# Optimization experiments

Measured on AMD Instinct MI355X. Metric: run time of the kernel, lower is better.

Reference implementation:

```python
import jax, jax.numpy as jnp
import numpy as np
import math

HEADS, LANDMARKS, PINV_ITERS, RES_K = 8, 256, 6, 33
DIM = 512


def layer_norm(x, g, b, eps=1e-5):
    mu = x.mean(-1, keepdims=True)
    var = ((x - mu) ** 2).mean(-1, keepdims=True)
    return (x - mu) * jax.lax.rsqrt(var + eps) * g + b


def iter_pinv(x, iters=PINV_ITERS):
    # Moore-Penrose pseudo-inverse via Newton-Schulz-like iteration (lucidrains nystrom-attention)
    ax = jnp.abs(x)
    z = jnp.swapaxes(x, -1, -2) / (jnp.max(ax.sum(-1)) * jnp.max(ax.sum(-2)))
    I = jnp.eye(x.shape[-1], dtype=x.dtype)
    for _ in range(iters):
        xz = x @ z
        z = 0.25 * z @ (13.0 * I - xz @ (15.0 * I - xz @ (7.0 * I - xz)))
    return z


def nystrom_attention(x, qkv_w, out_w, out_b, res_w):
    b, n, dim = x.shape
    h, m = HEADS, LANDMARKS
    d = dim // h
    pad = (m - n % m) % m
    xp = jnp.pad(x, ((0, 0), (pad, 0), (0, 0)))  # pad at sequence start (as in original)
    npad = n + pad
    qkv = xp @ qkv_w  # [b, npad, 3*dim]
    q, k, v = jnp.split(qkv, 3, axis=-1)
    q, k, v = (t.reshape(b, npad, h, d).transpose(0, 2, 1, 3) for t in (q, k, v))
    q = q * (d ** -0.5)
    l = npad // m
    q_l = q.reshape(b, h, m, l, d).mean(3)  # [b,h,m,d] landmarks
    k_l = k.reshape(b, h, m, l, d).mean(3)
    attn1 = jax.nn.softmax(jnp.einsum('bhid,bhjd->bhij', q, k_l), axis=-1)    # [b,h,npad,m]
    attn2 = jax.nn.softmax(jnp.einsum('bhid,bhjd->bhij', q_l, k_l), axis=-1)  # [b,h,m,m]
    attn3 = jax.nn.softmax(jnp.einsum('bhid,bhjd->bhij', q_l, k), axis=-1)    # [b,h,m,npad]
    out = (attn1 @ iter_pinv(attn2)) @ (attn3 @ v)  # [b,h,npad,d]
    # depthwise residual conv over sequence dim: v as NCHW = [b, heads, npad, d], kernel (33,1)
    res = jax.lax.conv_general_dilated(
        v, res_w, window_strides=(1, 1), padding=((RES_K // 2, RES_K // 2), (0, 0)),
        dimension_numbers=('NCHW', 'OIHW', 'NCHW'), feature_group_count=h)
    out = out + res
    out = out.transpose(0, 2, 1, 3).reshape(b, npad, dim)
    out = out @ out_w + out_b  # dropout is identity at eval
    return out[:, -n:]


def dwconv(x, w, b, k):
    y = jax.lax.conv_general_dilated(
        x, w, (1, 1), ((k // 2, k // 2), (k // 2, k // 2)),
        dimension_numbers=('NCHW', 'OIHW', 'NCHW'), feature_group_count=x.shape[1])
    return y + b[None, :, None, None]


def ppeg(x, H, W, w7, b7, w5, b5, w3, b3):
    B, _, C = x.shape
    cls_tok, feat = x[:, :1], x[:, 1:]
    cnn = feat.transpose(0, 2, 1).reshape(B, C, H, W)
    y = cnn + dwconv(cnn, w7, b7, 7) + dwconv(cnn, w5, b5, 5) + dwconv(cnn, w3, b3, 3)
    y = y.reshape(B, C, H * W).transpose(0, 2, 1)
    return jnp.concatenate([cls_tok, y], axis=1)


def _forward(features, fc1_w, fc1_b, cls_token,
             l1_norm_g, l1_norm_b, l1_qkv_w, l1_out_w, l1_out_b, l1_res_w,
             ppeg_w7, ppeg_b7, ppeg_w5, ppeg_b5, ppeg_w3, ppeg_b3,
             l2_norm_g, l2_norm_b, l2_qkv_w, l2_out_w, l2_out_b, l2_res_w,
             norm_g, norm_b, fc2_w, fc2_b):
    h = jax.nn.relu(features @ fc1_w + fc1_b)  # [B, N, 512]
    B, N, D = h.shape
    _H = _W = int(math.ceil(math.sqrt(N)))
    add_length = _H * _W - N
    h = jnp.concatenate([h, h[:, :add_length, :]], axis=1)  # square pad by wraparound
    h = jnp.concatenate([jnp.broadcast_to(cls_token, (B, 1, D)), h], axis=1)
    h = h + nystrom_attention(layer_norm(h, l1_norm_g, l1_norm_b), l1_qkv_w, l1_out_w, l1_out_b, l1_res_w)
    h = ppeg(h, _H, _W, ppeg_w7, ppeg_b7, ppeg_w5, ppeg_b5, ppeg_w3, ppeg_b3)
    h = h + nystrom_attention(layer_norm(h, l2_norm_g, l2_norm_b), l2_qkv_w, l2_out_w, l2_out_b, l2_res_w)
    h = layer_norm(h, norm_g, norm_b)[:, 0]
    return h @ fc2_w + fc2_b  # [B, num_classes]


def setup_inputs() -> dict:
    key = jax.random.key(0)
    ks = jax.random.split(key, 32)
    B, N, F, D = 2, 16000, 1024, DIM
    s = 0.02
    def rn(k, shape, scale=s):
        return jax.random.normal(k, shape, dtype=jnp.float32) * scale
    inp = {
        'features': jax.random.normal(ks[0], (B, N, F), dtype=jnp.float32),
        'fc1_w': rn(ks[1], (F, D)), 'fc1_b': jnp.zeros((D,), jnp.float32),
        'cls_token': rn(ks[2], (1, 1, D), 1.0),
        'l1_norm_g': jnp.ones((D,), jnp.float32), 'l1_norm_b': jnp.zeros((D,), jnp.float32),
        'l1_qkv_w': rn(ks[3], (D, 3 * D)),
        'l1_out_w': rn(ks[4], (D, D)), 'l1_out_b': jnp.zeros((D,), jnp.float32),
        'l1_res_w': rn(ks[5], (HEADS, 1, RES_K, 1)),
        'ppeg_w7': rn(ks[6], (D, 1, 7, 7)), 'ppeg_b7': jnp.zeros((D,), jnp.float32),
        'ppeg_w5': rn(ks[7], (D, 1, 5, 5)), 'ppeg_b5': jnp.zeros((D,), jnp.float32),
        'ppeg_w3': rn(ks[8], (D, 1, 3, 3)), 'ppeg_b3': jnp.zeros((D,), jnp.float32),
        'l2_norm_g': jnp.ones((D,), jnp.float32), 'l2_norm_b': jnp.zeros((D,), jnp.float32),
        'l2_qkv_w': rn(ks[9], (D, 3 * D)),
        'l2_out_w': rn(ks[10], (D, D)), 'l2_out_b': jnp.zeros((D,), jnp.float32),
        'l2_res_w': rn(ks[11], (HEADS, 1, RES_K, 1)),
        'norm_g': jnp.ones((D,), jnp.float32), 'norm_b': jnp.zeros((D,), jnp.float32),
        'fc2_w': rn(ks[12], (D, 1)), 'fc2_b': jnp.zeros((1,), jnp.float32),
    }
    return inp


def reference(features, fc1_w, fc1_b, cls_token,
              l1_norm_g, l1_norm_b, l1_qkv_w, l1_out_w, l1_out_b, l1_res_w,
              ppeg_w7, ppeg_b7, ppeg_w5, ppeg_b5, ppeg_w3, ppeg_b3,
              l2_norm_g, l2_norm_b, l2_qkv_w, l2_out_w, l2_out_b, l2_res_w,
              norm_g, norm_b, fc2_w, fc2_b):
    return _forward(features, fc1_w, fc1_b, cls_token,
                    l1_norm_g, l1_norm_b, l1_qkv_w, l1_out_w, l1_out_b, l1_res_w,
                    ppeg_w7, ppeg_b7, ppeg_w5, ppeg_b5, ppeg_w3, ppeg_b3,
                    l2_norm_g, l2_norm_b, l2_qkv_w, l2_out_w, l2_out_b, l2_res_w,
                    norm_g, norm_b, fc2_w, fc2_b)
```

## Files before the change

### kernel.cpp

```cpp
#include <hip/hip_runtime.h>
#include <math.h>

#define NTOK 16130
#define NPAD 16384
#define PADF 254
#define NB   2
#define DM   512
#define NH   8
#define HD   64
#define LM   256
#define SEG  64

typedef __attribute__((ext_vector_type(8))) short short8v;
typedef __attribute__((ext_vector_type(4))) float f32x4;

__device__ __forceinline__ float wred_max(float v){
  #pragma unroll
  for(int o=32;o;o>>=1) v=fmaxf(v,__shfl_xor(v,o));
  return v;
}
__device__ __forceinline__ float wred_sum(float v){
  #pragma unroll
  for(int o=32;o;o>>=1) v+=__shfl_xor(v,o);
  return v;
}
__device__ __forceinline__ float block_max256(float v, float* s4){
  v=wred_max(v);
  if((threadIdx.x&63)==0) s4[threadIdx.x>>6]=v;
  __syncthreads();
  v=fmaxf(fmaxf(s4[0],s4[1]),fmaxf(s4[2],s4[3]));
  __syncthreads();
  return v;
}
__device__ __forceinline__ float block_sum256(float v, float* s4){
  v=wred_sum(v);
  if((threadIdx.x&63)==0) s4[threadIdx.x>>6]=v;
  __syncthreads();
  v=s4[0]+s4[1]+s4[2]+s4[3];
  __syncthreads();
  return v;
}
__device__ __forceinline__ unsigned short f2bf(float f){
  unsigned u=__float_as_uint(f);
  u = u + 0x7FFFu + ((u>>16)&1u);
  return (unsigned short)(u>>16);
}
__device__ __forceinline__ float bf2f(unsigned short u){
  return __uint_as_float(((unsigned)u)<<16);
}
__device__ __forceinline__ unsigned cvtpk(float a, float b){
  unsigned r;
  asm("v_cvt_pk_bf16_f32 %0, %1, %2" : "=v"(r) : "v"(a), "v"(b));
  return r;
}

__global__ void k_wconv_t(const float* __restrict__ W, unsigned short* __restrict__ Wt,
                          int K, int N){
  int idx=blockIdx.x*256+threadIdx.x; if(idx>=K*N) return;
  int k=idx/N, n=idx%N;
  Wt[(size_t)n*K+k]=f2bf(W[idx]);
}

template<int MODE, int ASRC>
__global__ __launch_bounds__(256) void k_mfma_gemm(
    const void* __restrict__ Ap, const unsigned short* __restrict__ Bt,
    int M, int N, int K,
    const float* __restrict__ bias,
    void* __restrict__ o0, void* __restrict__ o1, void* __restrict__ o2)
{
  __shared__ unsigned short As[128*32];
  __shared__ unsigned short Bs[128*32];
  int t=threadIdx.x;
  int bx=blockIdx.x, by=blockIdx.y;
  {
    int gx=gridDim.x; int wg=by*gx+bx; int nwg=gx*gridDim.y;
    int cpx=nwg>>3; int x2=(wg&7)*cpx+(wg>>3);
    by=x2/gx; bx=x2-by*gx;
  }
  int row0=by*128, col0=bx*128;
  int lane=t&63, w=t>>6, wr=w>>1, wc=w&1, lr=lane&15, kg=lane>>4;
  f32x4 acc[4][4];
  #pragma unroll
  for(int m=0;m<4;m++)
    #pragma unroll
    for(int n=0;n<4;n++) acc[m][n]=(f32x4){0.f,0.f,0.f,0.f};

  auto loadA=[&](int r,int kofs)->short8v{
    if constexpr(ASRC==0){
      return *(const short8v*)((const unsigned short*)Ap+(size_t)(row0+r)*K+kofs);
    } else if constexpr(ASRC==1){
      const float* Af=(const float*)Ap;
      float4 f0=*(const float4*)(Af+(size_t)(row0+r)*K+kofs);
      float4 f1=*(const float4*)(Af+(size_t)(row0+r)*K+kofs+4);
      union{unsigned u[4]; short8v v;} pk;
      pk.u[0]=cvtpk(f0.x,f0.y); pk.u[1]=cvtpk(f0.z,f0.w);
      pk.u[2]=cvtpk(f1.x,f1.y); pk.u[3]=cvtpk(f1.z,f1.w);
      return pk.v;
    } else {
      const float* Af=(const float*)Ap;
      int rr2=row0+r; int bb=rr2>>14, ri=rr2&16383;
      int head=kofs>>6, dd=kofs&63;
      const float* p=Af + (((size_t)bb*NH+head)*NPAD+ri)*HD + dd;
      float4 f0=*(const float4*)p;
      float4 f1=*(const float4*)(p+4);
      union{unsigned u[4]; short8v v;} pk;
      pk.u[0]=cvtpk(f0.x,f0.y); pk.u[1]=cvtpk(f0.z,f0.w);
      pk.u[2]=cvtpk(f1.x,f1.y); pk.u[3]=cvtpk(f1.z,f1.w);
      return pk.v;
    }
  };

  short8v ra[2], rb[2];
  #pragma unroll
  for(int i=0;i<2;i++){
    int flat=i*256+t, r=flat>>2, k8=flat&3;
    ra[i]=loadA(r, k8*8);
    rb[i]=*(const short8v*)(Bt+(size_t)(col0+r)*K + k8*8);
  }
  int k0=0;
  for(;;){
    __syncthreads();
    #pragma unroll
    for(int i=0;i<2;i++){
      int flat=i*256+t;
      *(short8v*)(As+flat*8)=ra[i];
      *(short8v*)(Bs+flat*8)=rb[i];
    }
    __syncthreads();
    k0+=32;
    if(k0<K){
      #pragma unroll
      for(int i=0;i<2;i++){
        int flat=i*256+t, r=flat>>2, k8=flat&3;
        ra[i]=loadA(r, k0+k8*8);
        rb[i]=*(const short8v*)(Bt+(size_t)(col0+r)*K + k0 + k8*8);
      }
    }
    short8v af[4], bf[4];
    #pragma unroll
    for(int m=0;m<4;m++) af[m]=*(const short8v*)(As+(wr*64+m*16+lr)*32 + kg*8);
    #pragma unroll
    for(int n=0;n<4;n++) bf[n]=*(const short8v*)(Bs+(wc*64+n*16+lr)*32 + kg*8);
    #pragma unroll
    for(int m=0;m<4;m++)
      #pragma unroll
      for(int n=0;n<4;n++)
        acc[m][n]=__builtin_amdgcn_mfma_f32_16x16x32_bf16(af[m],bf[n],acc[m][n],0,0,0);
    if(k0>=K) break;
  }
  #pragma unroll
  for(int m=0;m<4;m++){
    int rbase=row0 + wr*64 + m*16 + kg*4;
    #pragma unroll
    for(int j=0;j<4;j++){
      int r=rbase+j;
      #pragma unroll
      for(int n=0;n<4;n++){
        int c=col0 + wc*64 + n*16 + lr;
        float val=acc[m][n][j];
        if(MODE==0){
          float* h=(float*)o0;
          int bb=(r>=16000)?1:0, ii=r-bb*16000;
          float vv=fmaxf(val+bias[c],0.f);
          h[((size_t)bb*NTOK + 1 + ii)*DM + c]=vv;
          if(ii<129) h[((size_t)bb*NTOK + 16001 + ii)*DM + c]=vv;
        } else if(MODE==1){
          int bb=r>>14, rr=r&16383;
          int which=c>>9, hcol=c&511, head=hcol>>6, dd=hcol&63;
          size_t o=(((size_t)bb*NH+head)*NPAD + rr)*HD + dd;
          if(which==0)      ((unsigned short*)o0)[o]=f2bf(val*0.125f);
          else if(which==1) ((unsigned short*)o1)[o]=f2bf(val);
          else              ((unsigned short*)o2)[o]=f2bf(val);
        } else {
          float* h=(float*)o0;
          int bb=r>>14, rr=r&16383;
          if(rr>=PADF)
            h[((size_t)bb*NTOK + (rr-PADF))*DM + c]+=val+bias[c];
        }
      }
    }
  }
}

__global__ void k_cls(const float* __restrict__ cls, float* __restrict__ h){
  int t=blockIdx.x*256+threadIdx.x;
  if(t<2*DM) h[(size_t)(t>>9)*NTOK*DM + (t&511)]=cls[t&511];
}

__global__ __launch_bounds__(256) void k_lnpad(
    const float* __restrict__ h, const float* __restrict__ g,
    const float* __restrict__ bta, unsigned short* __restrict__ xln)
{
  int r=blockIdx.x;
  int bb=r>>14, i=r&16383;
  int t=threadIdx.x;
  unsigned short* dst=xln+(size_t)r*DM;
  if(i<PADF){ dst[t]=0; dst[t+256]=0; return; }
  const float* src=h+((size_t)bb*NTOK + (i-PADF))*DM;
  float x0=src[t], x1=src[t+256];
  __shared__ float s4[4];
  float mu=block_sum256(x0+x1,s4)*(1.f/512.f);
  float d0=x0-mu, d1=x1-mu;
  float var=block_sum256(d0*d0+d1*d1,s4)*(1.f/512.f);
  float rst=rsqrtf(var+1e-5f);
  dst[t]    =f2bf(d0*rst*g[t]    +bta[t]);
  dst[t+256]=f2bf(d1*rst*g[t+256]+bta[t+256]);
}

__global__ void k_lmean2(const unsigned short* __restrict__ qsrc,
                         const unsigned short* __restrict__ ksrc,
                         float* __restrict__ qlf, unsigned short* __restrict__ qlb_,
                         float* __restrict__ klf, unsigned short* __restrict__ klb_){
  int gid=blockIdx.x;
  const unsigned short* src; float* dstf; unsigned short* dstb;
  if(gid<4096){ src=qsrc; dstf=qlf; dstb=qlb_; }
  else        { src=ksrc; dstf=klf; dstb=klb_; gid-=4096; }
  int bh=gid>>8, s=gid&255, d=threadIdx.x;
  const unsigned short* p=src + (((size_t)bh*NPAD)+s*SEG)*HD + d;
  float acc=0.f;
  #pragma unroll
  for(int l=0;l<SEG;l++) acc+=bf2f(p[(size_t)l*HD]);
  float m=acc*(1.f/64.f);
  dstf[((size_t)bh*LM+s)*HD+d]=m;
  dstb[((size_t)bh*LM+s)*HD+d]=f2bf(m);
}

__global__ __launch_bounds__(256) void k_vtrans(
    const unsigned short* __restrict__ v, unsigned short* __restrict__ vt)
{
  __shared__ unsigned short tile[64][72];
  int kt=blockIdx.x, bh=blockIdx.y;
  int t=threadIdx.x;
  int r=t>>2, sgq=t&3;
  const short8v* src=(const short8v*)(v + ((size_t)bh*NPAD + kt*64 + r)*HD + sgq*16);
  *(short8v*)(&tile[r][sgq*16])  =src[0];
  *(short8v*)(&tile[r][sgq*16+8])=src[1];
  __syncthreads();
  int d=t>>2;
  union{unsigned short u[16]; short8v v8[2];} pk;
  #pragma unroll
  for(int i=0;i<16;i++) pk.u[i]=tile[sgq*16+i][d];
  short8v* dst=(short8v*)(vt + ((size_t)bh*HD + d)*NPAD + kt*64 + sgq*16);
  dst[0]=pk.v8[0]; dst[1]=pk.v8[1];
}

__global__ __launch_bounds__(256) void k_attn2(
    const float* __restrict__ ql, const float* __restrict__ kl,
    float* __restrict__ attn2,
    unsigned short* __restrict__ a2h, unsigned short* __restrict__ a2l)
{
  __shared__ float qrow[64]; __shared__ float s4[4];
  int bh=blockIdx.x>>8, i=blockIdx.x&255, j=threadIdx.x;
  if(j<64) qrow[j]=ql[((size_t)bh*LM+i)*HD+j];
  __syncthreads();
  const float* kp=kl+((size_t)bh*LM+j)*HD;
  float l=0.f;
  #pragma unroll
  for(int d=0;d<64;d++) l+=qrow[d]*kp[d];
  float m=block_max256(l,s4);
  float e=__expf(l-m);
  float s=block_sum256(e,s4);
  float pv=e/s;
  size_t o=((size_t)bh*LM+i)*LM+j;
  attn2[o]=pv;
  unsigned short hh=f2bf(pv);
  a2h[o]=hh; a2l[o]=f2bf(pv-bf2f(hh));
}

__global__ void k_colsum(const float* __restrict__ x, float* __restrict__ cs){
  int bh=blockIdx.x, j=threadIdx.x;
  const float* p=x+(size_t)bh*65536;
  float s=0.f;
  for(int i=0;i<256;i++) s+=p[(size_t)i*256+j];
  cs[bh*256+j]=s;
}
__global__ void k_pinvscale(const float* __restrict__ cs, float* __restrict__ scale){
  __shared__ float s4[4];
  float mc=-1e30f;
  for(int i=threadIdx.x;i<4096;i+=256) mc=fmaxf(mc,cs[i]);
  mc=block_max256(mc,s4);
  if(threadIdx.x==0) scale[0]=1.f/mc;
}
__global__ void k_zinit_hl(const float* __restrict__ x, const float* __restrict__ scale,
    unsigned short* __restrict__ zh, unsigned short* __restrict__ zl,
    unsigned short* __restrict__ zth, unsigned short* __restrict__ ztl){
  int bh=blockIdx.x>>8, i=blockIdx.x&255, j=threadIdx.x;
  float s=scale[0];
  size_t base=(size_t)bh*65536;
  float vn=x[base+(size_t)j*256+i]*s;
  float vt=x[base+(size_t)i*256+j]*s;
  size_t o=base+(size_t)i*256+j;
  unsigned short h=f2bf(vn); zh[o]=h; zl[o]=f2bf(vn-bf2f(h));
  h=f2bf(vt); zth[o]=h; ztl[o]=f2bf(vt-bf2f(h));
}

template<int MODE, int PREC>
__global__ __launch_bounds__(256) void k_bmm3(
    const unsigned short* __restrict__ Ah, const unsigned short* __restrict__ Al,
    const unsigned short* __restrict__ Bth, const unsigned short* __restrict__ Btl,
    const unsigned short* __restrict__ Xh, const unsigned short* __restrict__ Xl,
    unsigned short* __restrict__ Cnh, unsigned short* __restrict__ Cnl,
    unsigned short* __restrict__ Cth, unsigned short* __restrict__ Ctl,
    int Ndim)
{
  __shared__ unsigned short AsH[64*40], BsH[64*40];
  __shared__ unsigned short AsL[PREC?64*40:8], BsL[PREC?64*40:8];
  int bh=blockIdx.z;
  int n0=blockIdx.x*64, m0=blockIdx.y*64;
  int t=threadIdx.x, lane=t&63, w=t>>6;
  int c=lane&15, g=lane>>4;
  int wr=(w>>1)*32, wc=(w&1)*32;
  f32x4 acc[2][2];
  #pragma unroll
  for(int i=0;i<2;i++)
    #pragma unroll
    for(int j=0;j<2;j++) acc[i][j]=(f32x4){0.f,0.f,0.f,0.f};
  size_t Abase=(size_t)bh*65536;
  size_t Bbase=(size_t)bh*(size_t)Ndim*256;
  int r=t>>2, sg=t&3;
  const unsigned short* Aptr=Ah +Abase+(size_t)(m0+r)*256+sg*8;
  const unsigned short* Bptr=Bth+Bbase+(size_t)(n0+r)*256+sg*8;
  const unsigned short* Alptr=Al +Abase+(size_t)(m0+r)*256+sg*8;
  const unsigned short* Blptr=Btl+Bbase+(size_t)(n0+r)*256+sg*8;
  short8v rah, rbh, ral, rbl;
  rah=*(const short8v*)(Aptr);
  rbh=*(const short8v*)(Bptr);
  if constexpr(PREC==1){ ral=*(const short8v*)(Alptr); rbl=*(const short8v*)(Blptr); }
  int k0=0;
  for(;;){
    __syncthreads();
    *(short8v*)(AsH+r*40+sg*8)=rah;
    *(short8v*)(BsH+r*40+sg*8)=rbh;
    if constexpr(PREC==1){
      *(short8v*)(AsL+r*40+sg*8)=ral;
      *(short8v*)(BsL+r*40+sg*8)=rbl;
    }
    __syncthreads();
    int kn=k0+32;
    if(kn<256){
      rah=*(const short8v*)(Aptr+kn);
      rbh=*(const short8v*)(Bptr+kn);
      if constexpr(PREC==1){
        ral=*(const short8v*)(Alptr+kn);
        rbl=*(const short8v*)(Blptr+kn);
      }
    }
    short8v bhf[2], blf[2];
    #pragma unroll
    for(int nt=0;nt<2;nt++){
      bhf[nt]=*(const short8v*)(BsH+(wc+nt*16+c)*40+g*8);
      if constexpr(PREC==1) blf[nt]=*(const short8v*)(BsL+(wc+nt*16+c)*40+g*8);
    }
    #pragma unroll
    for(int mt=0;mt<2;mt++){
      short8v ahh=*(const short8v*)(AsH+(wr+mt*16+c)*40+g*8);
      short8v all;
      if constexpr(PREC==1) all=*(const short8v*)(AsL+(wr+mt*16+c)*40+g*8);
      #pragma unroll
      for(int nt=0;nt<2;nt++){
        acc[mt][nt]=__builtin_amdgcn_mfma_f32_16x16x32_bf16(ahh,bhf[nt],acc[mt][nt],0,0,0);
        if constexpr(PREC==1){
          acc[mt][nt]=__builtin_amdgcn_mfma_f32_16x16x32_bf16(ahh,blf[nt],acc[mt][nt],0,0,0);
          acc[mt][nt]=__builtin_amdgcn_mfma_f32_16x16x32_bf16(all,bhf[nt],acc[mt][nt],0,0,0);
        }
      }
    }
    if(kn>=256) break;
    k0=kn;
  }
  #pragma unroll
  for(int mt=0;mt<2;mt++)
    #pragma unroll
    for(int nt=0;nt<2;nt++){
      int rb=m0+wr+mt*16+g*4;
      int cc=n0+wc+nt*16+c;
      float vv[4];
      #pragma unroll
      for(int j=0;j<4;j++){
        float a=acc[mt][nt][j];
        int rr=rb+j;
        if(MODE==1){
          float xv=bf2f(Xh[Abase+(size_t)rr*256+cc])+bf2f(Xl[Abase+(size_t)rr*256+cc]);
          a=(rr==cc?15.f:0.f)-7.f*xv+a;
        } else if(MODE==2){
          a=(rr==cc?13.f:0.f)-a;
        } else if(MODE==3){
          a*=0.25f;
        }
        vv[j]=a;
      }
      if(MODE==0||MODE==3){
        #pragma unroll
        for(int j=0;j<4;j++){
          unsigned short h=f2bf(vv[j]);
          Cnh[Abase+(size_t)(rb+j)*256+cc]=h;
          Cnl[Abase+(size_t)(rb+j)*256+cc]=f2bf(vv[j]-bf2f(h));
        }
      }
      {
        ushort4 hv, lv;
        hv.x=f2bf(vv[0]); hv.y=f2bf(vv[1]); hv.z=f2bf(vv[2]); hv.w=f2bf(vv[3]);
        lv.x=f2bf(vv[0]-bf2f(hv.x)); lv.y=f2bf(vv[1]-bf2f(hv.y));
        lv.z=f2bf(vv[2]-bf2f(hv.z)); lv.w=f2bf(vv[3]-bf2f(hv.w));
        size_t co=((size_t)bh*Ndim+cc)*256+rb;
        *(ushort4*)(Cth+co)=hv;
        if(MODE!=4) *(ushort4*)(Ctl+co)=lv;
      }
    }
}

__global__ __launch_bounds__(512) void k_attn3m(
    const unsigned short* __restrict__ qlb,
    const unsigned short* __restrict__ kb,
    const unsigned short* __restrict__ vtb,
    float* __restrict__ pacc, float* __restrict__ pms)
{
  __shared__ unsigned short Ks[64*72];
  __shared__ unsigned short Vs[64*72];
  int ck=blockIdx.x, bh=blockIdx.y;
  int t=threadIdx.x, lane=t&63, w=t>>6;
  int c=lane&15, g=lane>>4;
  short8v Qf[2][2];
  #pragma unroll
  for(int n=0;n<2;n++)
    #pragma unroll
    for(int kw=0;kw<2;kw++)
      Qf[n][kw]=*(const short8v*)(qlb + ((size_t)bh*LM + w*32 + n*16 + c)*HD + kw*32 + g*8);
  f32x4 accO[4][2];
  float mrun[2], srun[2];
  #pragma unroll
  for(int n=0;n<2;n++){
    mrun[n]=-3e38f; srun[n]=0.f;
    #pragma unroll
    for(int d=0;d<4;d++) accO[d][n]=(f32x4){0.f,0.f,0.f,0.f};
  }
  int sr=t>>3, sgk=t&7;
  for(int sc=0;sc<16;++sc){
    int key0=ck*1024 + sc*64;
    __syncthreads();
    *(short8v*)(Ks + sr*72 + sgk*8) =
      *(const short8v*)(kb + ((size_t)bh*NPAD + key0 + sr)*HD + sgk*8);
    *(short8v*)(Vs + sr*72 + sgk*8) =
      *(const short8v*)(vtb + ((size_t)bh*HD + sr)*NPAD + key0 + sgk*8);
    __syncthreads();
    f32x4 s[4][2];
    #pragma unroll
    for(int mt=0;mt<4;mt++){
      short8v a0=*(const short8v*)(Ks + (mt*16+c)*72 + g*8);
      short8v a1=*(const short8v*)(Ks + (mt*16+c)*72 + 32 + g*8);
      #pragma unroll
      for(int n=0;n<2;n++){
        f32x4 z=(f32x4){0.f,0.f,0.f,0.f};
        z=__builtin_amdgcn_mfma_f32_16x16x32_bf16(a0,Qf[n][0],z,0,0,0);
        z=__builtin_amdgcn_mfma_f32_16x16x32_bf16(a1,Qf[n][1],z,0,0,0);
        s[mt][n]=z;
      }
    }
    unsigned U[2][4][2];
    #pragma unroll
    for(int n=0;n<2;n++){
      float cm=-3e38f;
      #pragma unroll
      for(int mt=0;mt<4;mt++)
        #pragma unroll
        for(int j=0;j<4;j++) cm=fmaxf(cm,s[mt][n][j]);
      cm=fmaxf(cm,__shfl_xor(cm,16));
      cm=fmaxf(cm,__shfl_xor(cm,32));
      float mnew=fmaxf(mrun[n],cm);
      float f=__expf(mrun[n]-mnew);
      mrun[n]=mnew;
      float ps=0.f;
      #pragma unroll
      for(int mt=0;mt<4;mt++){
        float p0=__expf(s[mt][n][0]-mnew);
        float p1=__expf(s[mt][n][1]-mnew);
        float p2=__expf(s[mt][n][2]-mnew);
        float p3=__expf(s[mt][n][3]-mnew);
        ps+=p0+p1+p2+p3;
        U[n][mt][0]=cvtpk(p0,p1);
        U[n][mt][1]=cvtpk(p2,p3);
      }
      ps+=__shfl_xor(ps,16); ps+=__shfl_xor(ps,32);
      srun[n]=srun[n]*f+ps;
      #pragma unroll
      for(int d=0;d<4;d++){
        accO[d][n][0]*=f; accO[d][n][1]*=f; accO[d][n][2]*=f; accO[d][n][3]*=f;
      }
    }
    #pragma unroll
    for(int kw=0;kw<2;kw++){
      short8v pf[2];
      #pragma unroll
      for(int n=0;n<2;n++){
        union{unsigned u[4]; short8v v;} pk;
        #pragma unroll
        for(int wd=0;wd<4;wd++){
          int sl=c+16*(((g&1)<<1)+(wd>>1));
          unsigned va=(unsigned)__shfl((int)U[n][kw*2  ][wd&1],sl);
          unsigned vb=(unsigned)__shfl((int)U[n][kw*2+1][wd&1],sl);
          pk.u[wd]=(lane>=32)?vb:va;
        }
        pf[n]=pk.v;
      }
      #pragma unroll
      for(int d=0;d<4;d++){
        short8v vf=*(const short8v*)(Vs + (d*16+c)*72 + kw*32 + g*8);
        accO[d][0]=__builtin_amdgcn_mfma_f32_16x16x32_bf16(vf,pf[0],accO[d][0],0,0,0);
        accO[d][1]=__builtin_amdgcn_mfma_f32_16x16x32_bf16(vf,pf[1],accO[d][1],0,0,0);
      }
    }
  }
  size_t pb=((size_t)bh*16+ck)*LM;
  #pragma unroll
  for(int n=0;n<2;n++){
    int q=w*32+n*16+c;
    #pragma unroll
    for(int d=0;d<4;d++)
      *(f32x4*)(pacc + (pb+q)*HD + d*16 + g*4)=accO[d][n];
    if(g==0){ pms[(pb+q)*2]=mrun[n]; pms[(pb+q)*2+1]=srun[n]; }
  }
}
__global__ __launch_bounds__(256) void k_attn3vc(
    const float* __restrict__ pacc, const float* __restrict__ pms,
    unsigned short* __restrict__ a3vth, unsigned short* __restrict__ a3vtl)
{
  int gid=blockIdx.x*4+(threadIdx.x>>6);
  int bh=gid>>8, row=gid&255, lane=threadIdx.x&63;
  float M=-3e38f;
  float ms[16], ss[16];
  #pragma unroll
  for(int c=0;c<16;c++){
    size_t pb=((size_t)bh*16+c)*LM+row;
    ms[c]=pms[pb*2]; ss[c]=pms[pb*2+1];
    M=fmaxf(M,ms[c]);
  }
  float S=0.f,a=0.f;
  #pragma unroll
  for(int c=0;c<16;c++){
    float f=__expf(ms[c]-M);
    S+=ss[c]*f;
    a+=pacc[(((size_t)bh*16+c)*LM+row)*HD+lane]*f;
  }
  float v=a/S;
  unsigned short hi=f2bf(v);
  a3vth[((size_t)bh*HD+lane)*LM+row]=hi;
  a3vtl[((size_t)bh*HD+lane)*LM+row]=f2bf(v-bf2f(hi));
}

__global__ __launch_bounds__(512) void k_attn1m(
    const unsigned short* __restrict__ qb,
    const unsigned short* __restrict__ klb,
    const unsigned short* __restrict__ w2t,
    float* __restrict__ aoh)
{
  __shared__ unsigned short klS[256*72];
  __shared__ unsigned short w2S[64*264];
  int qt=blockIdx.x, bh=blockIdx.y;
  int t=threadIdx.x, lane=t&63, w=t>>6;
  int c=lane&15, g=lane>>4;
  {
    int r=t>>1, hf=t&1;
    const short8v* s=(const short8v*)(klb + ((size_t)bh*LM+r)*HD + hf*32);
    short8v* d=(short8v*)(klS + r*72 + hf*32);
    d[0]=s[0]; d[1]=s[1]; d[2]=s[2]; d[3]=s[3];
    int r2=t>>3, sg2=t&7;
    const short8v* s2=(const short8v*)(w2t + ((size_t)bh*HD+r2)*LM + sg2*32);
    short8v* d2=(short8v*)(w2S + r2*264 + sg2*32);
    d2[0]=s2[0]; d2[1]=s2[1]; d2[2]=s2[2]; d2[3]=s2[3];
  }
  __syncthreads();
  int q0=qt*256 + w*32;
  #pragma unroll
  for(int n=0;n<2;n++){
    const unsigned short* qrow=qb + ((size_t)bh*NPAD + q0 + n*16 + c)*HD;
    short8v qf0=*(const short8v*)(qrow + g*8);
    short8v qf1=*(const short8v*)(qrow + 32 + g*8);
    f32x4 s[16];
    #pragma unroll
    for(int mt=0;mt<16;mt++){
      short8v a0=*(const short8v*)(klS + (mt*16+c)*72 + g*8);
      short8v a1=*(const short8v*)(klS + (mt*16+c)*72 + 32 + g*8);
      f32x4 z=(f32x4){0.f,0.f,0.f,0.f};
      z=__builtin_amdgcn_mfma_f32_16x16x32_bf16(a0,qf0,z,0,0,0);
      z=__builtin_amdgcn_mfma_f32_16x16x32_bf16(a1,qf1,z,0,0,0);
      s[mt]=z;
    }
    float M=-3e38f;
    #pragma unroll
    for(int mt=0;mt<16;mt++)
      #pragma unroll
      for(int j=0;j<4;j++) M=fmaxf(M,s[mt][j]);
    M=fmaxf(M,__shfl_xor(M,16));
    M=fmaxf(M,__shfl_xor(M,32));
    float sum=0.f;
    unsigned U[16][2];
    #pragma unroll
    for(int mt=0;mt<16;mt++){
      float p0=__expf(s[mt][0]-M);
      float p1=__expf(s[mt][1]-M);
      float p2=__expf(s[mt][2]-M);
      float p3=__expf(s[mt][3]-M);
      sum+=p0+p1+p2+p3;
      U[mt][0]=cvtpk(p0,p1);
      U[mt][1]=cvtpk(p2,p3);
    }
    sum+=__shfl_xor(sum,16); sum+=__shfl_xor(sum,32);
    float inv=1.f/sum;
    f32x4 accO[4];
    #pragma unroll
    for(int d=0;d<4;d++) accO[d]=(f32x4){0.f,0.f,0.f,0.f};
    #pragma unroll
    for(int kw=0;kw<8;kw++){
      union{unsigned u[4]; short8v v;} pk;
      #pragma unroll
      for(int wd=0;wd<4;wd++){
        int sl=c+16*(((g&1)<<1)+(wd>>1));
        unsigned va=(unsigned)__shfl((int)U[kw*2  ][wd&1],sl);
        unsigned vb=(unsigned)__shfl((int)U[kw*2+1][wd&1],sl);
        pk.u[wd]=(lane>=32)?vb:va;
      }
      #pragma unroll
      for(int d=0;d<4;d++){
        short8v vf=*(const short8v*)(w2S + (d*16+c)*264 + kw*32 + g*8);
        accO[d]=__builtin_amdgcn_mfma_f32_16x16x32_bf16(vf,pk.v,accO[d],0,0,0);
      }
    }
    int q=q0+n*16+c;
    #pragma unroll
    for(int d=0;d<4;d++){
      f32x4 o=accO[d];
      o[0]*=inv; o[1]*=inv; o[2]*=inv; o[3]*=inv;
      *(f32x4*)(aoh + ((size_t)bh*NPAD+q)*HD + d*16 + g*4)=o;
    }
  }
}

__global__ __launch_bounds__(256) void k_resconv2(
    const unsigned short* __restrict__ vt, const float* __restrict__ rw,
    float* __restrict__ aoh){
  int bx=blockIdx.x, bh=blockIdx.y;
  int t=threadIdx.x, d=t&63, g=t>>6;
  int i0=bx*32+g*8;
  int hh=bh&7;
  const unsigned short* vr=vt + ((size_t)bh*HD + d)*NPAD;
  float wv[40];
  int start=i0-16;
  if(start>=0 && start+40<=NPAD){
    #pragma unroll
    for(int b=0;b<5;b++){
      short8v v8=*(const short8v*)(vr+start+b*8);
      #pragma unroll
      for(int j=0;j<8;j++) wv[b*8+j]=bf2f((unsigned short)v8[j]);
    }
  } else {
    #pragma unroll
    for(int t2=0;t2<40;t2++){
      int src=start+t2;
      wv[t2]=(src>=0&&src<NPAD)?bf2f(vr[src]):0.f;
    }
  }
  const float* wt=rw+hh*33;
  #pragma unroll
  for(int p=0;p<8;p++){
    float a=0.f;
    #pragma unroll
    for(int tk=0;tk<33;tk++) a+=wv[p+tk]*wt[tk];
    aoh[((size_t)bh*NPAD+i0+p)*HD+d]+=a;
  }
}

__global__ void k_wprep(const float* __restrict__ w7, const float* __restrict__ b7,
                        const float* __restrict__ w5, const float* __restrict__ b5,
                        const float* __restrict__ w3, const float* __restrict__ b3,
                        unsigned short* __restrict__ wcat){
  int t=blockIdx.x*256+threadIdx.x;
  if(t>=50*512) return;
  int r=t>>9, c=t&511;
  float v;
  if(r<49){
    int ky=r/7, kx=r%7;
    v=w7[(size_t)c*49+r];
    if(ky>=1&&ky<=5&&kx>=1&&kx<=5) v+=w5[(size_t)c*25+(ky-1)*5+(kx-1)];
    if(ky>=2&&ky<=4&&kx>=2&&kx<=4) v+=w3[(size_t)c*9+(ky-2)*3+(kx-2)];
  } else {
    v=b7[c]+b5[c]+b3[c];
  }
  wcat[t]=f2bf(v);
}

__global__ __launch_bounds__(256,4) void k_ppeg4(
    const float* __restrict__ src, const unsigned short* __restrict__ wcat,
    float* __restrict__ dst)
{
  __shared__ float patch[196][32];
  __shared__ float wsf[50][32];
  int bx=blockIdx.x;
  int cz=blockIdx.y, bb=blockIdx.z;
  int t=threadIdx.x, c=t&31, g=t>>5;
  int ty0=(bx>>4)*8, tx0=(bx&15)*8;
  const float* base=src+((size_t)bb*NTOK+1)*DM + cz*32 + c;
  #pragma unroll
  for(int i=0;i<25;i++){
    int p=g+8*i;
    if(p<196){
      int py=p/14, px=p%14;
      int yy=ty0-3+py, xx=tx0-3+px;
      float v=0.f;
      if(yy>=0&&yy<127&&xx>=0&&xx<127) v=base[(size_t)(yy*127+xx)*DM];
      patch[p][c]=v;
    }
  }
  #pragma unroll
  for(int i=0;i<7;i++){
    int r=g+8*i; if(r<50) wsf[r][c]=bf2f(wcat[(size_t)r*DM + cz*32 + c]);
  }
  __syncthreads();
  float acc[8];
  float bias=wsf[49][c];
  #pragma unroll
  for(int j=0;j<8;j++) acc[j]=patch[(g+3)*14+(j+3)][c]+bias;
  #pragma unroll
  for(int ky=0;ky<7;ky++){
    float win[14];
    #pragma unroll
    for(int x=0;x<14;x++) win[x]=patch[(g+ky)*14+x][c];
    #pragma unroll
    for(int kx=0;kx<7;kx++){
      float wv=wsf[ky*7+kx][c];
      #pragma unroll
      for(int j=0;j<8;j++) acc[j]+=win[j+kx]*wv;
    }
  }
  int y=ty0+g;
  if(y<127){
    #pragma unroll
    for(int j=0;j<8;j++){
      int x=tx0+j;
      if(x<127)
        dst[((size_t)bb*NTOK+1+(size_t)(y*127+x))*DM + cz*32 + c]=acc[j];
    }
  }
}

__global__ void k_cpcls(const float* __restrict__ h, float* __restrict__ dst){
  int t=blockIdx.x*256+threadIdx.x;
  if(t<2*DM) dst[(size_t)(t>>9)*NTOK*DM + (t&511)]=h[(size_t)(t>>9)*NTOK*DM + (t&511)];
}

__global__ __launch_bounds__(256) void k_final(
    const float* __restrict__ h, const float* __restrict__ g, const float* __restrict__ bta,
    const float* __restrict__ w, const float* __restrict__ fb, float* __restrict__ out)
{
  int bb=blockIdx.x, t=threadIdx.x;
  const float* src=h+(size_t)bb*NTOK*DM;
  float x0=src[t], x1=src[t+256];
  __shared__ float s4[4];
  float mu=block_sum256(x0+x1,s4)*(1.f/512.f);
  float d0=x0-mu, d1=x1-mu;
  float var=block_sum256(d0*d0+d1*d1,s4)*(1.f/512.f);
  float rst=rsqrtf(var+1e-5f);
  float y0=d0*rst*g[t]+bta[t], y1=d1*rst*g[t+256]+bta[t+256];
  float dot=block_sum256(y0*w[t]+y1*w[t+256],s4);
  if(t==0) out[bb]=dot+fb[0];
}

extern "C" void kernel_launch(void* const* d_in, const int* in_sizes, int n_in,
                              void* d_out, int out_size, void* d_ws, size_t ws_size,
                              hipStream_t stream){
  (void)in_sizes; (void)n_in; (void)out_size; (void)ws_size;
  const float* features=(const float*)d_in[0];
  const float* fc1_w  =(const float*)d_in[1];
  const float* fc1_b  =(const float*)d_in[2];
  const float* cls_tok=(const float*)d_in[3];
  const float* fc2_w  =(const float*)d_in[24];
  const float* fc2_b  =(const float*)d_in[25];
  float* out=(float*)d_out;

  char* wp=(char*)d_ws;
  auto allocB=[&](size_t bytes)->char*{
    char* p=wp; wp+=((bytes+255)/256)*256; return p;
  };
  float* h    =(float*)allocB((size_t)NB*NTOK*DM*4);
  float* h2   =(float*)allocB((size_t)NB*NTOK*DM*4);
  unsigned short* vb  =(unsigned short*)allocB((size_t)NB*NPAD*DM*2);
  unsigned short* xlnb=(unsigned short*)allocB((size_t)NB*NPAD*DM*2);
  unsigned short* qb  =(unsigned short*)allocB((size_t)NB*NPAD*DM*2);
  unsigned short* kb  =(unsigned short*)allocB((size_t)NB*NPAD*DM*2);
  unsigned short* vtb =(unsigned short*)allocB((size_t)NB*NPAD*DM*2);
  float* aoh  =(float*)allocB((size_t)NB*NPAD*DM*4);
  unsigned short* wtf=(unsigned short*)allocB((size_t)512*1024*2);
  unsigned short* wtq=(unsigned short*)allocB((size_t)1536*512*2);
  unsigned short* wtp=(unsigned short*)allocB((size_t)512*512*2);
  float* ql =(float*)allocB((size_t)16*LM*HD*4);
  float* kl =(float*)allocB((size_t)16*LM*HD*4);
  unsigned short* qlb=(unsigned short*)allocB((size_t)16*LM*HD*2);
  unsigned short* klb=(unsigned short*)allocB((size_t)16*LM*HD*2);
  float* attn2=(float*)allocB((size_t)16*LM*LM*4);
  unsigned short* a2h=(unsigned short*)allocB((size_t)16*LM*LM*2);
  unsigned short* a2l=(unsigned short*)allocB((size_t)16*LM*LM*2);
  unsigned short* zb[8];
  for(int i=0;i<8;i++) zb[i]=(unsigned short*)allocB((size_t)16*LM*LM*2);
  unsigned short* Abh=(unsigned short*)allocB((size_t)16*LM*LM*2);
  unsigned short* Abl=(unsigned short*)allocB((size_t)16*LM*LM*2);
  unsigned short* Abth=(unsigned short*)allocB((size_t)16*LM*LM*2);
  unsigned short* Abtl=(unsigned short*)allocB((size_t)16*LM*LM*2);
  unsigned short* Ubth=(unsigned short*)allocB((size_t)16*LM*LM*2);
  unsigned short* Ubtl=(unsigned short*)allocB((size_t)16*LM*LM*2);
  unsigned short* Tbth=(unsigned short*)allocB((size_t)16*LM*LM*2);
  unsigned short* Tbtl=(unsigned short*)allocB((size_t)16*LM*LM*2);
  unsigned short* a3vth=(unsigned short*)allocB((size_t)16*HD*LM*2);
  unsigned short* a3vtl=(unsigned short*)allocB((size_t)16*HD*LM*2);
  unsigned short* w2t=(unsigned short*)allocB((size_t)16*HD*LM*2);
  float* pacc=(float*)allocB((size_t)16*16*LM*HD*4);
  float* pms =(float*)allocB((size_t)16*16*LM*2*4);
  float* cs  =(float*)allocB(4096*4);
  float* scl =(float*)allocB(64*4);

  auto nystrom=[&](float* hbuf, const float* ng, const float* nbias, const float* qkvw,
                   const float* outw, const float* outb, const float* resw){
    k_lnpad<<<NB*NPAD,256,0,stream>>>(hbuf, ng, nbias, xlnb);
    k_wconv_t<<<(512*1536+255)/256,256,0,stream>>>(qkvw, wtq, 512, 1536);
    k_mfma_gemm<1,0><<<dim3(12,256),256,0,stream>>>(xlnb, wtq, 32768,1536,512,
                                                    nullptr, qb, kb, vb);
    k_lmean2<<<8192,64,0,stream>>>(qb, kb, ql, qlb, kl, klb);
    k_vtrans<<<dim3(256,16),256,0,stream>>>(vb, vtb);
    k_attn2<<<4096,256,0,stream>>>(ql, kl, attn2, a2h, a2l);
    k_colsum<<<16,256,0,stream>>>(attn2, cs);
    k_pinvscale<<<1,256,0,stream>>>(cs, scl);
    k_zinit_hl<<<4096,256,0,stream>>>(attn2, scl, zb[0],zb[1],zb[2],zb[3]);
    unsigned short *zch=zb[0],*zcl=zb[1],*zcth=zb[2],*zctl=zb[3];
    unsigned short *znh=zb[4],*znl=zb[5],*znth=zb[6],*zntl=zb[7];
    for(int it=0;it<6;it++){
      if(it<5){
        k_bmm3<0,0><<<dim3(4,4,16),256,0,stream>>>(a2h,a2l, zcth,zctl, nullptr,nullptr,
                                                   Abh,Abl, Abth,Abtl, 256);
        k_bmm3<1,0><<<dim3(4,4,16),256,0,stream>>>(Abh,Abl, Abth,Abtl, Abh,Abl,
                                                   nullptr,nullptr, Ubth,Ubtl, 256);
        k_bmm3<2,0><<<dim3(4,4,16),256,0,stream>>>(Abh,Abl, Ubth,Ubtl, nullptr,nullptr,
                                                   nullptr,nullptr, Tbth,Tbtl, 256);
        k_bmm3<3,0><<<dim3(4,4,16),256,0,stream>>>(zch,zcl, Tbth,Tbtl, nullptr,nullptr,
                                                   znh,znl, znth,zntl, 256);
      } else {
        k_bmm3<0,1><<<dim3(4,4,16),256,0,stream>>>(a2h,a2l, zcth,zctl, nullptr,nullptr,
                                                   Abh,Abl, Abth,Abtl, 256);
        k_bmm3<1,1><<<dim3(4,4,16),256,0,stream>>>(Abh,Abl, Abth,Abtl, Abh,Abl,
                                                   nullptr,nullptr, Ubth,Ubtl, 256);
        k_bmm3<2,1><<<dim3(4,4,16),256,0,stream>>>(Abh,Abl, Ubth,Ubtl, nullptr,nullptr,
                                                   nullptr,nullptr, Tbth,Tbtl, 256);
        k_bmm3<3,1><<<dim3(4,4,16),256,0,stream>>>(zch,zcl, Tbth,Tbtl, nullptr,nullptr,
                                                   znh,znl, znth,zntl, 256);
      }
      unsigned short* tp;
      tp=zch; zch=znh; znh=tp;  tp=zcl; zcl=znl; znl=tp;
      tp=zcth; zcth=znth; znth=tp;  tp=zctl; zctl=zntl; zntl=tp;
    }
    k_attn3m<<<dim3(16,16),512,0,stream>>>(qlb, kb, vtb, pacc, pms);
    k_attn3vc<<<1024,256,0,stream>>>(pacc, pms, a3vth, a3vtl);
    k_bmm3<4,1><<<dim3(1,4,16),256,0,stream>>>(zch,zcl, a3vth,a3vtl, nullptr,nullptr,
                                               nullptr,nullptr, w2t,nullptr, 64);
    k_attn1m<<<dim3(64,16),512,0,stream>>>(qb, klb, w2t, aoh);
    k_resconv2<<<dim3(512,16),256,0,stream>>>(vtb, resw, aoh);
    k_wconv_t<<<(512*512+255)/256,256,0,stream>>>(outw, wtp, 512, 512);
    k_mfma_gemm<2,2><<<dim3(4,256),256,0,stream>>>(aoh, wtp, 32768,512,512,
                                                   outb, hbuf, nullptr, nullptr);
  };

  k_wconv_t<<<(1024*512+255)/256,256,0,stream>>>(fc1_w, wtf, 1024, 512);
  k_mfma_gemm<0,1><<<dim3(4,250),256,0,stream>>>(features, wtf, 32000,512,1024,
                                                 fc1_b, h, nullptr, nullptr);
  k_cls<<<4,256,0,stream>>>(cls_tok, h);

  nystrom(h, (const float*)d_in[4],(const float*)d_in[5],(const float*)d_in[6],
          (const float*)d_in[7],(const float*)d_in[8],(const float*)d_in[9]);

  {
    unsigned short* wcat=(unsigned short*)attn2;
    k_wprep<<<100,256,0,stream>>>(
        (const float*)d_in[10],(const float*)d_in[11],
        (const float*)d_in[12],(const float*)d_in[13],
        (const float*)d_in[14],(const float*)d_in[15], wcat);
    k_cpcls<<<4,256,0,stream>>>(h, h2);
    k_ppeg4<<<dim3(256,16,2),256,0,stream>>>(h, wcat, h2);
  }

  nystrom(h2, (const float*)d_in[16],(const float*)d_in[17],(const float*)d_in[18],
          (const float*)d_in[19],(const float*)d_in[20],(const float*)d_in[21]);

  k_final<<<2,256,0,stream>>>(h2,(const float*)d_in[22],(const float*)d_in[23],
                              fc2_w, fc2_b, out);
}
```

Baseline: 1.345 ms.

## Use direct global-to-LDS loads in GEMM, pre-convert features, stage QKV epilogue

The bf16 GEMM now loads tiles straight into LDS with global_load_lds instead of staging them through registers. The register double-buffering for bf16 A is dropped, and only the fp32 head-layout A path keeps its register prefetch. The fc1 GEMM now reads features that a separate kernel first converts to bf16 in a scratch buffer, trading an extra full pass over the features for a cheaper GEMM inner loop. The QKV epilogue writes results through LDS so global stores become 16-byte vectors instead of scattered 2-byte stores.

```diff
diff --git a/kernel.cpp b/kernel.cpp
--- a/kernel.cpp
+++ b/kernel.cpp
@@ -13,6 +13,7 @@
 
 typedef __attribute__((ext_vector_type(8))) short short8v;
 typedef __attribute__((ext_vector_type(4))) float f32x4;
+typedef unsigned int u32;
 
 __device__ __forceinline__ float wred_max(float v){
   #pragma unroll
@@ -53,7 +54,18 @@
   asm("v_cvt_pk_bf16_f32 %0, %1, %2" : "=v"(r) : "v"(a), "v"(b));
   return r;
 }
-
+__device__ __forceinline__ void gl16(const unsigned short* g, unsigned short* l){
+  __builtin_amdgcn_global_load_lds(
+      (const __attribute__((address_space(1))) u32*)(g),
+      (__attribute__((address_space(3))) u32*)(l), 16, 0, 0);
+}
+
+__global__ void k_f2bf4(const float* __restrict__ x, unsigned short* __restrict__ y, int n4){
+  int i=blockIdx.x*256+threadIdx.x; if(i>=n4) return;
+  float4 v=((const float4*)x)[i];
+  ushort4 r; r.x=f2bf(v.x); r.y=f2bf(v.y); r.z=f2bf(v.z); r.w=f2bf(v.w);
+  ((ushort4*)y)[i]=r;
+}
 __global__ void k_wconv_t(const float* __restrict__ W, unsigned short* __restrict__ Wt,
                           int K, int N){
   int idx=blockIdx.x*256+threadIdx.x; if(idx>=K*N) return;
@@ -68,8 +80,7 @@
     const float* __restrict__ bias,
     void* __restrict__ o0, void* __restrict__ o1, void* __restrict__ o2)
 {
-  __shared__ unsigned short As[128*32];
-  __shared__ unsigned short Bs[128*32];
+  __shared__ __align__(16) unsigned short Sh[128*64];
   int t=threadIdx.x;
   int bx=blockIdx.x, by=blockIdx.y;
   {
@@ -85,97 +96,115 @@
     #pragma unroll
     for(int n=0;n<4;n++) acc[m][n]=(f32x4){0.f,0.f,0.f,0.f};
 
-  auto loadA=[&](int r,int kofs)->short8v{
+  auto loadA2=[&](int r,int kofs)->short8v{
+    const float* Af=(const float*)Ap;
+    int rr2=row0+r; int bb=rr2>>14, ri=rr2&16383;
+    int head=kofs>>6, dd=kofs&63;
+    const float* p=Af + (((size_t)bb*NH+head)*NPAD+ri)*HD + dd;
+    float4 f0=*(const float4*)p;
+    float4 f1=*(const float4*)(p+4);
+    union{unsigned u[4]; short8v v;} pk;
+    pk.u[0]=cvtpk(f0.x,f0.y); pk.u[1]=cvtpk(f0.z,f0.w);
+    pk.u[2]=cvtpk(f1.x,f1.y); pk.u[3]=cvtpk(f1.z,f1.w);
+    return pk.v;
+  };
+
+  short8v ra[2];
+  if constexpr(ASRC==2){
+    #pragma unroll
+    for(int i=0;i<2;i++){ int flat=i*256+t, r=flat>>2, k8=flat&3; ra[i]=loadA2(r, k8*8); }
+  }
+  for(int k0=0;k0<K;k0+=32){
+    __syncthreads();
     if constexpr(ASRC==0){
-      return *(const short8v*)((const unsigned short*)Ap+(size_t)(row0+r)*K+kofs);
-    } else if constexpr(ASRC==1){
-      const float* Af=(const float*)Ap;
-      float4 f0=*(const float4*)(Af+(size_t)(row0+r)*K+kofs);
-      float4 f1=*(const float4*)(Af+(size_t)(row0+r)*K+kofs+4);
-      union{unsigned u[4]; short8v v;} pk;
-      pk.u[0]=cvtpk(f0.x,f0.y); pk.u[1]=cvtpk(f0.z,f0.w);
-      pk.u[2]=cvtpk(f1.x,f1.y); pk.u[3]=cvtpk(f1.z,f1.w);
-      return pk.v;
-    } else {
-      const float* Af=(const float*)Ap;
-      int rr2=row0+r; int bb=rr2>>14, ri=rr2&16383;
-      int head=kofs>>6, dd=kofs&63;
-      const float* p=Af + (((size_t)bb*NH+head)*NPAD+ri)*HD + dd;
-      float4 f0=*(const float4*)p;
-      float4 f1=*(const float4*)(p+4);
-      union{unsigned u[4]; short8v v;} pk;
-      pk.u[0]=cvtpk(f0.x,f0.y); pk.u[1]=cvtpk(f0.z,f0.w);
-      pk.u[2]=cvtpk(f1.x,f1.y); pk.u[3]=cvtpk(f1.z,f1.w);
-      return pk.v;
-    }
-  };
-
-  short8v ra[2], rb[2];
-  #pragma unroll
-  for(int i=0;i<2;i++){
-    int flat=i*256+t, r=flat>>2, k8=flat&3;
-    ra[i]=loadA(r, k8*8);
-    rb[i]=*(const short8v*)(Bt+(size_t)(col0+r)*K + k8*8);
-  }
-  int k0=0;
-  for(;;){
-    __syncthreads();
-    #pragma unroll
-    for(int i=0;i<2;i++){
-      int flat=i*256+t;
-      *(short8v*)(As+flat*8)=ra[i];
-      *(short8v*)(Bs+flat*8)=rb[i];
-    }
-    __syncthreads();
-    k0+=32;
-    if(k0<K){
       #pragma unroll
       for(int i=0;i<2;i++){
         int flat=i*256+t, r=flat>>2, k8=flat&3;
-        ra[i]=loadA(r, k0+k8*8);
-        rb[i]=*(const short8v*)(Bt+(size_t)(col0+r)*K + k0 + k8*8);
-      }
-    }
+        gl16((const unsigned short*)Ap+(size_t)(row0+r)*K+k0+k8*8, Sh+(size_t)flat*8);
+        gl16(Bt+(size_t)(col0+r)*K+k0+k8*8, Sh+4096+(size_t)flat*8);
+      }
+    } else {
+      #pragma unroll
+      for(int i=0;i<2;i++){
+        int flat=i*256+t;
+        *(short8v*)(Sh+(size_t)flat*8)=ra[i];
+        int r=flat>>2, k8=flat&3;
+        gl16(Bt+(size_t)(col0+r)*K+k0+k8*8, Sh+4096+(size_t)flat*8);
+      }
+      if(k0+32<K){
+        #pragma unroll
+        for(int i=0;i<2;i++){ int flat=i*256+t, r=flat>>2, k8=flat&3; ra[i]=loadA2(r, k0+32+k8*8); }
+      }
+    }
+    __syncthreads();
     short8v af[4], bf[4];
     #pragma unroll
-    for(int m=0;m<4;m++) af[m]=*(const short8v*)(As+(wr*64+m*16+lr)*32 + kg*8);
-    #pragma unroll
-    for(int n=0;n<4;n++) bf[n]=*(const short8v*)(Bs+(wc*64+n*16+lr)*32 + kg*8);
+    for(int m=0;m<4;m++) af[m]=*(const short8v*)(Sh+(wr*64+m*16+lr)*32 + kg*8);
+    #pragma unroll
+    for(int n=0;n<4;n++) bf[n]=*(const short8v*)(Sh+4096+(wc*64+n*16+lr)*32 + kg*8);
     #pragma unroll
     for(int m=0;m<4;m++)
       #pragma unroll
       for(int n=0;n<4;n++)
         acc[m][n]=__builtin_amdgcn_mfma_f32_16x16x32_bf16(af[m],bf[n],acc[m][n],0,0,0);
-    if(k0>=K) break;
-  }
-  #pragma unroll
-  for(int m=0;m<4;m++){
-    int rbase=row0 + wr*64 + m*16 + kg*4;
-    #pragma unroll
-    for(int j=0;j<4;j++){
-      int r=rbase+j;
-      #pragma unroll
-      for(int n=0;n<4;n++){
-        int c=col0 + wc*64 + n*16 + lr;
-        float val=acc[m][n][j];
-        if(MODE==0){
-          float* h=(float*)o0;
-          int bb=(r>=16000)?1:0, ii=r-bb*16000;
-          float vv=fmaxf(val+bias[c],0.f);
-          h[((size_t)bb*NTOK + 1 + ii)*DM + c]=vv;
-          if(ii<129) h[((size_t)bb*NTOK + 16001 + ii)*DM + c]=vv;
-        } else if(MODE==1){
-          int bb=r>>14, rr=r&16383;
-          int which=c>>9, hcol=c&511, head=hcol>>6, dd=hcol&63;
-          size_t o=(((size_t)bb*NH+head)*NPAD + rr)*HD + dd;
-          if(which==0)      ((unsigned short*)o0)[o]=f2bf(val*0.125f);
-          else if(which==1) ((unsigned short*)o1)[o]=f2bf(val);
-          else              ((unsigned short*)o2)[o]=f2bf(val);
-        } else {
-          float* h=(float*)o0;
-          int bb=r>>14, rr=r&16383;
-          if(rr>=PADF)
-            h[((size_t)bb*NTOK + (rr-PADF))*DM + c]+=val+bias[c];
+  }
+  if constexpr(MODE==1){
+    #pragma unroll
+    for(int p=0;p<2;p++){
+      __syncthreads();
+      #pragma unroll
+      for(int mm=0;mm<2;mm++){
+        int m=2*p+mm;
+        #pragma unroll
+        for(int n=0;n<4;n++){
+          int cc=wc*64+n*16+lr;
+          int c=col0+cc;
+          float sc=((c>>9)==0)?0.125f:1.f;
+          #pragma unroll
+          for(int j=0;j<4;j++){
+            int lrow=wr*32+mm*16+kg*4+j;
+            Sh[lrow*128+cc]=f2bf(acc[m][n][j]*sc);
+          }
+        }
+      }
+      __syncthreads();
+      #pragma unroll
+      for(int i=0;i<4;i++){
+        int p2=i*256+t;
+        int r2=p2>>4, ck=p2&15;
+        int grow=row0+(r2>>5)*64+(2*p+((r2>>4)&1))*16+(r2&15);
+        int bb=grow>>14, rr=grow&16383;
+        int c=col0+ck*8;
+        int which=c>>9, hcol=c&511, head=hcol>>6, dd=hcol&63;
+        unsigned short* dst=(which==0)?(unsigned short*)o0:
+                            (which==1)?(unsigned short*)o1:(unsigned short*)o2;
+        *(short8v*)(dst + (((size_t)bb*NH+head)*NPAD+rr)*HD+dd) =
+            *(const short8v*)(Sh + r2*128 + ck*8);
+      }
+    }
+  } else {
+    #pragma unroll
+    for(int m=0;m<4;m++){
+      int rbase=row0 + wr*64 + m*16 + kg*4;
+      #pragma unroll
+      for(int j=0;j<4;j++){
+        int r=rbase+j;
+        #pragma unroll
+        for(int n=0;n<4;n++){
+          int c=col0 + wc*64 + n*16 + lr;
+          float val=acc[m][n][j];
+          if(MODE==0){
+            float* h=(float*)o0;
+            int bb=(r>=16000)?1:0, ii=r-bb*16000;
+            float vv=fmaxf(val+bias[c],0.f);
+            h[((size_t)bb*NTOK + 1 + ii)*DM + c]=vv;
+            if(ii<129) h[((size_t)bb*NTOK + 16001 + ii)*DM + c]=vv;
+          } else {
+            float* h=(float*)o0;
+            int bb=r>>14, rr=r&16383;
+            if(rr>=PADF)
+              h[((size_t)bb*NTOK + (rr-PADF))*DM + c]+=val+bias[c];
+          }
         }
       }
     }
@@ -865,8 +894,10 @@
                                                    outb, hbuf, nullptr, nullptr);
   };
 
+  unsigned short* featbf=(unsigned short*)h2;
+  k_f2bf4<<<32000,256,0,stream>>>(features, featbf, 32000*1024/4);
   k_wconv_t<<<(1024*512+255)/256,256,0,stream>>>(fc1_w, wtf, 1024, 512);
-  k_mfma_gemm<0,1><<<dim3(4,250),256,0,stream>>>(features, wtf, 32000,512,1024,
+  k_mfma_gemm<0,0><<<dim3(4,250),256,0,stream>>>(featbf, wtf, 32000,512,1024,
                                                  fc1_b, h, nullptr, nullptr);
   k_cls<<<4,256,0,stream>>>(cls_tok, h);
 
```

Measured after the change: 1.358 ms. No clear change (+1.0%).
